# Kernel tuning notes

Hardware: AMD Instinct MI355X
Metric: run time of the kernel (lower is better)

## Reference

```python
import jax, jax.numpy as jnp
import numpy as np

IMG = 224      # image height/width
P = 4          # patch size
R = 16         # number of superpixels (SLIC num_segments)
B = 32         # batch
D = 768        # embed dim


def setup_inputs() -> dict:
    key = jax.random.key(0)
    k1, k2 = jax.random.split(key)
    n_patches = (IMG // P) ** 2  # 3136
    patch_embeddings = jax.random.normal(k1, (B, n_patches, D), dtype=jnp.float32)
    segmentation_map = jax.random.randint(k2, (B, IMG, IMG), 0, R, dtype=jnp.int32)
    return {
        "patch_embeddings": patch_embeddings,
        "segmentation_map": segmentation_map,
        "patch_size": P,
        "num_segments": R,
    }


def _dominant_segment_ids(segmentation_map, patch_size, num_segments):
    # Vectorized PatchToSuperpixelMapper.map_patches: per-patch mode of labels.
    Bm, H, W = segmentation_map.shape
    npx = H // patch_size
    # [B, npx, p, npx, p] -> [B, N, p*p] pixels per patch
    pix = (segmentation_map
           .reshape(Bm, npx, patch_size, npx, patch_size)
           .transpose(0, 1, 3, 2, 4)
           .reshape(Bm, npx * npx, patch_size * patch_size))
    # histogram over segment labels; argmax tie-breaks to smallest label,
    # matching torch.unique (sorted) + counts.argmax.
    counts = jnp.sum(pix[..., None] == jnp.arange(num_segments, dtype=pix.dtype), axis=2)  # [B, N, R]
    return jnp.argmax(counts, axis=-1)  # [B, N] int


def reference(patch_embeddings, segmentation_map, patch_size, num_segments):
    # SuperpixelPooling('mean').pool driven by map_patches, fully vectorized.
    Bm, N, Dm = patch_embeddings.shape
    seg_ids = _dominant_segment_ids(segmentation_map, patch_size, num_segments)  # [B, N]
    # offset segment ids per batch element -> single segment_sum over B*R bins
    flat_ids = (seg_ids + jnp.arange(Bm, dtype=seg_ids.dtype)[:, None] * num_segments).reshape(-1)
    sums = jax.ops.segment_sum(patch_embeddings.reshape(Bm * N, Dm), flat_ids,
                               num_segments=Bm * num_segments)            # [B*R, D]
    cnt = jax.ops.segment_sum(jnp.ones((Bm * N,), patch_embeddings.dtype), flat_ids,
                              num_segments=Bm * num_segments)             # [B*R]
    pooled = sums / jnp.maximum(cnt, 1.0)[:, None]  # empty superpixels stay zero
    return pooled.reshape(Bm, num_segments, Dm)
```

## Files before the change

kernel.cpp:

```cpp
#include <hip/hip_runtime.h>

#define IMG 224
#define PSZ 4
#define NPX (IMG / PSZ)
#define NPATCH (NPX * NPX)
#define BB 32
#define RR 16
#define DD 768
#define NCHUNK 16
#define CHUNK (NPATCH / NCHUNK)
#define T2 192

__global__ __launch_bounds__(256) void k_segids(const int* __restrict__ seg,
                                                int* __restrict__ seg_ids,
                                                int* __restrict__ counts) {
    int t = blockIdx.x * 256 + threadIdx.x;
    if (t >= BB * NPATCH) return;
    int b = t / NPATCH;
    int n = t - b * NPATCH;
    int py = n / NPX, px = n - py * NPX;
    const int* base = seg + ((size_t)b * IMG + (size_t)py * PSZ) * IMG + px * PSZ;
    unsigned long long lo = 0ull, hi = 0ull;
#pragma unroll
    for (int i = 0; i < PSZ; i++) {
        int4 v = *(const int4*)(base + (size_t)i * IMG);
        int ss[4] = {v.x, v.y, v.z, v.w};
#pragma unroll
        for (int j = 0; j < 4; j++) {
            int s = ss[j];
            unsigned long long inc = 1ull << ((s & 7) * 8);
            if (s < 8) lo += inc; else hi += inc;
        }
    }
    int best = 0, bc = -1;
#pragma unroll
    for (int r = 0; r < RR; r++) {
        unsigned long long word = (r < 8) ? lo : hi;
        int c = (int)((word >> ((r & 7) * 8)) & 0xffull);
        if (c > bc) { bc = c; best = r; }
    }
    seg_ids[t] = best;
    atomicAdd(&counts[b * RR + best], 1);
}

template <bool ATOMIC>
__global__ __launch_bounds__(T2) void k_pool(const float* __restrict__ emb,
                                             const int* __restrict__ seg_ids,
                                             float* __restrict__ dst) {
    const int blk = blockIdx.x;
    const int b = blk / NCHUNK;
    const int c = blk - b * NCHUNK;
    const int n0 = c * CHUNK;
    __shared__ int sseg[CHUNK];
    for (int i = threadIdx.x; i < CHUNK; i += T2)
        sseg[i] = seg_ids[b * NPATCH + n0 + i];
    __syncthreads();

    const int t = threadIdx.x;
    const float* src = emb + ((size_t)(b * NPATCH + n0)) * DD + t * 4;

    float4 acc[RR];
#pragma unroll
    for (int r = 0; r < RR; r++) acc[r] = make_float4(0.f, 0.f, 0.f, 0.f);

    for (int p = 0; p < CHUNK; p += 4) {
        float4 v0 = *(const float4*)(src + (size_t)(p + 0) * DD);
        float4 v1 = *(const float4*)(src + (size_t)(p + 1) * DD);
        float4 v2 = *(const float4*)(src + (size_t)(p + 2) * DD);
        float4 v3 = *(const float4*)(src + (size_t)(p + 3) * DD);
        int s0 = sseg[p + 0], s1 = sseg[p + 1], s2 = sseg[p + 2], s3 = sseg[p + 3];
#pragma unroll
        for (int r = 0; r < RR; r++) {
            float w0 = (s0 == r) ? 1.f : 0.f;
            float w1 = (s1 == r) ? 1.f : 0.f;
            float w2 = (s2 == r) ? 1.f : 0.f;
            float w3 = (s3 == r) ? 1.f : 0.f;
            acc[r].x = fmaf(w0, v0.x, acc[r].x);
            acc[r].y = fmaf(w0, v0.y, acc[r].y);
            acc[r].z = fmaf(w0, v0.z, acc[r].z);
            acc[r].w = fmaf(w0, v0.w, acc[r].w);
            acc[r].x = fmaf(w1, v1.x, acc[r].x);
            acc[r].y = fmaf(w1, v1.y, acc[r].y);
            acc[r].z = fmaf(w1, v1.z, acc[r].z);
            acc[r].w = fmaf(w1, v1.w, acc[r].w);
            acc[r].x = fmaf(w2, v2.x, acc[r].x);
            acc[r].y = fmaf(w2, v2.y, acc[r].y);
            acc[r].z = fmaf(w2, v2.z, acc[r].z);
            acc[r].w = fmaf(w2, v2.w, acc[r].w);
            acc[r].x = fmaf(w3, v3.x, acc[r].x);
            acc[r].y = fmaf(w3, v3.y, acc[r].y);
            acc[r].z = fmaf(w3, v3.z, acc[r].z);
            acc[r].w = fmaf(w3, v3.w, acc[r].w);
        }
    }

    if (ATOMIC) {
        float* o = dst + ((size_t)b * RR) * DD + t * 4;
#pragma unroll
        for (int r = 0; r < RR; r++) {
            atomicAdd(o + r * DD + 0, acc[r].x);
            atomicAdd(o + r * DD + 1, acc[r].y);
            atomicAdd(o + r * DD + 2, acc[r].z);
            atomicAdd(o + r * DD + 3, acc[r].w);
        }
    } else {
        float* o = dst + (((size_t)c * BB + b) * RR) * DD + t * 4;
#pragma unroll
        for (int r = 0; r < RR; r++)
            *(float4*)(o + r * DD) = acc[r];
    }
}

__global__ __launch_bounds__(256) void k_finish_part(const float* __restrict__ part,
                                                     const int* __restrict__ counts,
                                                     float* __restrict__ out) {
    int e = blockIdx.x * 256 + threadIdx.x;
    if (e >= BB * RR * DD) return;
    float s = 0.f;
#pragma unroll
    for (int c = 0; c < NCHUNK; c++) s += part[(size_t)c * (BB * RR * DD) + e];
    int br = e / DD;
    float cnt = (float)counts[br];
    out[e] = s / fmaxf(cnt, 1.f);
}

__global__ __launch_bounds__(256) void k_finish_atomic(const int* __restrict__ counts,
                                                       float* __restrict__ out) {
    int e = blockIdx.x * 256 + threadIdx.x;
    if (e >= BB * RR * DD) return;
    int br = e / DD;
    float cnt = (float)counts[br];
    out[e] = out[e] / fmaxf(cnt, 1.f);
}

extern "C" void kernel_launch(void* const* d_in, const int* in_sizes, int n_in,
                              void* d_out, int out_size, void* d_ws, size_t ws_size,
                              hipStream_t stream) {
    const float* emb = (const float*)d_in[0];
    const int* segmap = (const int*)d_in[1];
    (void)in_sizes; (void)n_in; (void)out_size;

    char* ws = (char*)d_ws;
    int* seg_ids = (int*)ws;
    int* counts = (int*)(ws + 401408);
    float* part = (float*)(ws + 403456);
    const size_t need = 403456 + (size_t)NCHUNK * BB * RR * DD * sizeof(float);
    float* out = (float*)d_out;

    hipMemsetAsync(counts, 0, BB * RR * sizeof(int), stream);
    k_segids<<<(BB * NPATCH + 255) / 256, 256, 0, stream>>>(segmap, seg_ids, counts);

    if (ws_size >= need) {
        k_pool<false><<<BB * NCHUNK, T2, 0, stream>>>(emb, seg_ids, part);
        k_finish_part<<<(BB * RR * DD + 255) / 256, 256, 0, stream>>>(part, counts, out);
    } else {
        hipMemsetAsync(out, 0, (size_t)BB * RR * DD * sizeof(float), stream);
        k_pool<true><<<BB * NCHUNK, T2, 0, stream>>>(emb, seg_ids, out);
        k_finish_atomic<<<(BB * RR * DD + 255) / 256, 256, 0, stream>>>(counts, out);
    }
}
```

Measured before the change: 449.6 us.

## Fuse segment-id computation into pooling kernel and double chunk count

Removes the separate segment-id kernel: each pooling block now computes the dominant label for its own patches directly from the segmentation map, keeps per-block counts in shared memory and adds them to global counts with one atomic per label. The chunk count goes from 16 to 32, which doubles the number of blocks for parallelism; the main loop is left un-unrolled and gets a tail for the odd chunk size of 98. The finish kernel is rewritten to use float4 per block row. Costs include more partial-sum traffic (twice the partial buffer) and redundant-free but serialized label work at block start.

```diff
diff --git a/kernel.cpp b/kernel.cpp
--- a/kernel.cpp
+++ b/kernel.cpp
@@ -7,54 +7,54 @@
 #define BB 32
 #define RR 16
 #define DD 768
-#define NCHUNK 16
+#define NCHUNK 32
 #define CHUNK (NPATCH / NCHUNK)
 #define T2 192
 
-__global__ __launch_bounds__(256) void k_segids(const int* __restrict__ seg,
-                                                int* __restrict__ seg_ids,
-                                                int* __restrict__ counts) {
-    int t = blockIdx.x * 256 + threadIdx.x;
-    if (t >= BB * NPATCH) return;
-    int b = t / NPATCH;
-    int n = t - b * NPATCH;
-    int py = n / NPX, px = n - py * NPX;
-    const int* base = seg + ((size_t)b * IMG + (size_t)py * PSZ) * IMG + px * PSZ;
-    unsigned long long lo = 0ull, hi = 0ull;
-#pragma unroll
-    for (int i = 0; i < PSZ; i++) {
-        int4 v = *(const int4*)(base + (size_t)i * IMG);
-        int ss[4] = {v.x, v.y, v.z, v.w};
-#pragma unroll
-        for (int j = 0; j < 4; j++) {
-            int s = ss[j];
-            unsigned long long inc = 1ull << ((s & 7) * 8);
-            if (s < 8) lo += inc; else hi += inc;
-        }
-    }
-    int best = 0, bc = -1;
-#pragma unroll
-    for (int r = 0; r < RR; r++) {
-        unsigned long long word = (r < 8) ? lo : hi;
-        int c = (int)((word >> ((r & 7) * 8)) & 0xffull);
-        if (c > bc) { bc = c; best = r; }
-    }
-    seg_ids[t] = best;
-    atomicAdd(&counts[b * RR + best], 1);
-}
-
 template <bool ATOMIC>
 __global__ __launch_bounds__(T2) void k_pool(const float* __restrict__ emb,
-                                             const int* __restrict__ seg_ids,
+                                             const int* __restrict__ segmap,
+                                             int* __restrict__ counts,
                                              float* __restrict__ dst) {
     const int blk = blockIdx.x;
     const int b = blk / NCHUNK;
     const int c = blk - b * NCHUNK;
     const int n0 = c * CHUNK;
+
     __shared__ int sseg[CHUNK];
-    for (int i = threadIdx.x; i < CHUNK; i += T2)
-        sseg[i] = seg_ids[b * NPATCH + n0 + i];
+    __shared__ int lcnt[RR];
+    if (threadIdx.x < RR) lcnt[threadIdx.x] = 0;
     __syncthreads();
+
+    for (int i = threadIdx.x; i < CHUNK; i += T2) {
+        int n = n0 + i;
+        int py = n / NPX, px = n - py * NPX;
+        const int* base = segmap + ((size_t)b * IMG + (size_t)py * PSZ) * IMG + px * PSZ;
+        unsigned long long lo = 0ull, hi = 0ull;
+#pragma unroll
+        for (int j = 0; j < PSZ; j++) {
+            int4 v = *(const int4*)(base + (size_t)j * IMG);
+            int ss[4] = {v.x, v.y, v.z, v.w};
+#pragma unroll
+            for (int k = 0; k < 4; k++) {
+                int s = ss[k];
+                unsigned long long inc = 1ull << ((s & 7) * 8);
+                if (s < 8) lo += inc; else hi += inc;
+            }
+        }
+        int best = 0, bc = -1;
+#pragma unroll
+        for (int r = 0; r < RR; r++) {
+            unsigned long long word = (r < 8) ? lo : hi;
+            int cc = (int)((word >> ((r & 7) * 8)) & 0xffull);
+            if (cc > bc) { bc = cc; best = r; }
+        }
+        sseg[i] = best;
+        atomicAdd(&lcnt[best], 1);
+    }
+    __syncthreads();
+    if (threadIdx.x < RR)
+        atomicAdd(&counts[b * RR + threadIdx.x], lcnt[threadIdx.x]);
 
     const int t = threadIdx.x;
     const float* src = emb + ((size_t)(b * NPATCH + n0)) * DD + t * 4;
@@ -63,7 +63,8 @@
 #pragma unroll
     for (int r = 0; r < RR; r++) acc[r] = make_float4(0.f, 0.f, 0.f, 0.f);
 
-    for (int p = 0; p < CHUNK; p += 4) {
+#pragma unroll 1
+    for (int p = 0; p < CHUNK - 2; p += 4) {
         float4 v0 = *(const float4*)(src + (size_t)(p + 0) * DD);
         float4 v1 = *(const float4*)(src + (size_t)(p + 1) * DD);
         float4 v2 = *(const float4*)(src + (size_t)(p + 2) * DD);
@@ -93,6 +94,25 @@
             acc[r].w = fmaf(w3, v3.w, acc[r].w);
         }
     }
+    {
+        const int p = CHUNK - 2;
+        float4 v0 = *(const float4*)(src + (size_t)(p + 0) * DD);
+        float4 v1 = *(const float4*)(src + (size_t)(p + 1) * DD);
+        int s0 = sseg[p + 0], s1 = sseg[p + 1];
+#pragma unroll
+        for (int r = 0; r < RR; r++) {
+            float w0 = (s0 == r) ? 1.f : 0.f;
+            float w1 = (s1 == r) ? 1.f : 0.f;
+            acc[r].x = fmaf(w0, v0.x, acc[r].x);
+            acc[r].y = fmaf(w0, v0.y, acc[r].y);
+            acc[r].z = fmaf(w0, v0.z, acc[r].z);
+            acc[r].w = fmaf(w0, v0.w, acc[r].w);
+            acc[r].x = fmaf(w1, v1.x, acc[r].x);
+            acc[r].y = fmaf(w1, v1.y, acc[r].y);
+            acc[r].z = fmaf(w1, v1.z, acc[r].z);
+            acc[r].w = fmaf(w1, v1.w, acc[r].w);
+        }
+    }
 
     if (ATOMIC) {
         float* o = dst + ((size_t)b * RR) * DD + t * 4;
@@ -111,25 +131,28 @@
     }
 }
 
-__global__ __launch_bounds__(256) void k_finish_part(const float* __restrict__ part,
-                                                     const int* __restrict__ counts,
-                                                     float* __restrict__ out) {
-    int e = blockIdx.x * 256 + threadIdx.x;
-    if (e >= BB * RR * DD) return;
-    float s = 0.f;
+__global__ __launch_bounds__(T2) void k_finish_part(const float* __restrict__ part,
+                                                    const int* __restrict__ counts,
+                                                    float* __restrict__ out) {
+    const int br = blockIdx.x;
+    const int t = threadIdx.x;
+    const float* p0 = part + (size_t)br * DD + t * 4;
+    float4 s = make_float4(0.f, 0.f, 0.f, 0.f);
 #pragma unroll
-    for (int c = 0; c < NCHUNK; c++) s += part[(size_t)c * (BB * RR * DD) + e];
-    int br = e / DD;
-    float cnt = (float)counts[br];
-    out[e] = s / fmaxf(cnt, 1.f);
+    for (int c = 0; c < NCHUNK; c++) {
+        float4 v = *(const float4*)(p0 + (size_t)c * (BB * RR * DD));
+        s.x += v.x; s.y += v.y; s.z += v.z; s.w += v.w;
+    }
+    float inv = 1.f / fmaxf((float)counts[br], 1.f);
+    float4 o = make_float4(s.x * inv, s.y * inv, s.z * inv, s.w * inv);
+    *(float4*)(out + (size_t)br * DD + t * 4) = o;
 }
 
 __global__ __launch_bounds__(256) void k_finish_atomic(const int* __restrict__ counts,
                                                        float* __restrict__ out) {
     int e = blockIdx.x * 256 + threadIdx.x;
     if (e >= BB * RR * DD) return;
-    int br = e / DD;
-    float cnt = (float)counts[br];
+    float cnt = (float)counts[e / DD];
     out[e] = out[e] / fmaxf(cnt, 1.f);
 }
 
@@ -141,21 +164,19 @@
     (void)in_sizes; (void)n_in; (void)out_size;
 
     char* ws = (char*)d_ws;
-    int* seg_ids = (int*)ws;
-    int* counts = (int*)(ws + 401408);
-    float* part = (float*)(ws + 403456);
-    const size_t need = 403456 + (size_t)NCHUNK * BB * RR * DD * sizeof(float);
+    int* counts = (int*)ws;
+    float* part = (float*)(ws + 2048);
+    const size_t need = 2048 + (size_t)NCHUNK * BB * RR * DD * sizeof(float);
     float* out = (float*)d_out;
 
     hipMemsetAsync(counts, 0, BB * RR * sizeof(int), stream);
-    k_segids<<<(BB * NPATCH + 255) / 256, 256, 0, stream>>>(segmap, seg_ids, counts);
 
     if (ws_size >= need) {
-        k_pool<false><<<BB * NCHUNK, T2, 0, stream>>>(emb, seg_ids, part);
-        k_finish_part<<<(BB * RR * DD + 255) / 256, 256, 0, stream>>>(part, counts, out);
+        k_pool<false><<<BB * NCHUNK, T2, 0, stream>>>(emb, segmap, counts, part);
+        k_finish_part<<<BB * RR, T2, 0, stream>>>(part, counts, out);
     } else {
         hipMemsetAsync(out, 0, (size_t)BB * RR * DD * sizeof(float), stream);
-        k_pool<true><<<BB * NCHUNK, T2, 0, stream>>>(emb, seg_ids, out);
+        k_pool<true><<<BB * NCHUNK, T2, 0, stream>>>(emb, segmap, counts, out);
         k_finish_atomic<<<(BB * RR * DD + 255) / 256, 256, 0, stream>>>(counts, out);
     }
 }
```

Result: faster. 437.9 us (-2.6%).
